# Kernel tuning notes

Hardware: AMD Instinct MI355X
Metric: run time of the kernel (lower is better)

## Reference

```python
import jax, jax.numpy as jnp
import numpy as np

D_MODEL = 1024
N_HEAD = 16
D_FF = 4 * D_MODEL
LN_EPS = 1e-5


def _layernorm(x, g, b):
    mu = jnp.mean(x, axis=-1, keepdims=True)
    var = jnp.mean(jnp.square(x - mu), axis=-1, keepdims=True)
    return (x - mu) * jax.lax.rsqrt(var + LN_EPS) * g + b


def _mha(q_in, k_in, v_in, mask, wq, bq, wk, wv, bv, wo, bo):
    B, Tq, D = q_in.shape
    H, Dk = N_HEAD, D // N_HEAD
    q = (q_in @ wq + bq).reshape(B, Tq, H, Dk).transpose(0, 2, 1, 3)      # [B,H,Tq,Dk]
    k = (k_in @ wk).reshape(B, -1, H, Dk).transpose(0, 2, 1, 3)           # [B,H,Tk,Dk]
    v = (v_in @ wv + bv).reshape(B, -1, H, Dk).transpose(0, 2, 1, 3)      # [B,H,Tk,Dk]
    attn = jnp.einsum('bhqd,bhkd->bhqk', q, k) / jnp.sqrt(jnp.float32(Dk))
    if mask is not None:
        m0 = (mask[:, None, :, :] == 0)                                    # [B,1,Tq,Tk]
        attn = jnp.where(m0, -jnp.inf, attn)
        attn = jax.nn.softmax(attn, axis=-1)
        attn = jnp.where(m0, 0.0, attn)
    else:
        attn = jax.nn.softmax(attn, axis=-1)
    out = jnp.einsum('bhqk,bhkd->bhqd', attn, v)
    out = out.transpose(0, 2, 1, 3).reshape(B, Tq, D)
    return out @ wo + bo


def setup_inputs() -> dict:
    key = jax.random.key(0)
    ks = jax.random.split(key, 32)
    B, T, S, D = 4, 1024, 1024, D_MODEL
    w = lambda k, shp: 0.02 * jax.random.normal(k, shp, dtype=jnp.float32)
    inp = {
        'dec_input': jax.random.normal(ks[0], (B, T, D), dtype=jnp.float32),
        'enc_output': jax.random.normal(ks[1], (B, S, D), dtype=jnp.float32),
        'self_mask': jnp.broadcast_to(jnp.tril(jnp.ones((T, T), jnp.int32)), (B, T, T)),
        'cross_mask': jnp.ones((B, T, S), jnp.int32),
        'sa_ln_g': jnp.ones((D,), jnp.float32), 'sa_ln_b': jnp.zeros((D,), jnp.float32),
        'sa_wq': w(ks[2], (D, D)), 'sa_bq': jnp.zeros((D,), jnp.float32),
        'sa_wk': w(ks[3], (D, D)),
        'sa_wv': w(ks[4], (D, D)), 'sa_bv': jnp.zeros((D,), jnp.float32),
        'sa_wo': w(ks[5], (D, D)), 'sa_bo': jnp.zeros((D,), jnp.float32),
        'ca_ln_g': jnp.ones((D,), jnp.float32), 'ca_ln_b': jnp.zeros((D,), jnp.float32),
        'ca_wq': w(ks[6], (D, D)), 'ca_bq': jnp.zeros((D,), jnp.float32),
        'ca_wk': w(ks[7], (D, D)),
        'ca_wv': w(ks[8], (D, D)), 'ca_bv': jnp.zeros((D,), jnp.float32),
        'ca_wo': w(ks[9], (D, D)), 'ca_bo': jnp.zeros((D,), jnp.float32),
        'mlp_ln_g': jnp.ones((D,), jnp.float32), 'mlp_ln_b': jnp.zeros((D,), jnp.float32),
        'w1': w(ks[10], (D, D_FF)), 'b1': jnp.zeros((D_FF,), jnp.float32),
        'w2': w(ks[11], (D_FF, D)), 'b2': jnp.zeros((D,), jnp.float32),
    }
    return inp


def reference(dec_input, enc_output, self_mask, cross_mask,
              sa_ln_g, sa_ln_b, sa_wq, sa_bq, sa_wk, sa_wv, sa_bv, sa_wo, sa_bo,
              ca_ln_g, ca_ln_b, ca_wq, ca_bq, ca_wk, ca_wv, ca_bv, ca_wo, ca_bo,
              mlp_ln_g, mlp_ln_b, w1, b1, w2, b2):
    # self-attention block (pre-norm, residual)
    x = _layernorm(dec_input, sa_ln_g, sa_ln_b)
    x = dec_input + _mha(x, x, x, self_mask, sa_wq, sa_bq, sa_wk, sa_wv, sa_bv, sa_wo, sa_bo)
    # cross-attention block
    h = _layernorm(x, ca_ln_g, ca_ln_b)
    x = x + _mha(h, enc_output, enc_output, cross_mask, ca_wq, ca_bq, ca_wk, ca_wv, ca_bv, ca_wo, ca_bo)
    # GELU FFN block
    h = _layernorm(x, mlp_ln_g, mlp_ln_b)
    x = x + (jax.nn.gelu(h @ w1 + b1, approximate=False) @ w2 + b2)
    return x
```

## Files before the change

### kernel.cpp

```cpp
#include <hip/hip_runtime.h>
#include <math.h>

typedef unsigned short u16;
typedef unsigned int   u32;
typedef __attribute__((ext_vector_type(8))) short bf16x8;
typedef __attribute__((ext_vector_type(4))) float f32x4;

__device__ __forceinline__ u16 f2bf(float f) {
  u32 u = __builtin_bit_cast(u32, f);
  u += 0x7fffu + ((u >> 16) & 1u);
  return (u16)(u >> 16);
}
__device__ __forceinline__ u32 cvtpk(float lo, float hi_) {
  u32 r;
  asm("v_cvt_pk_bf16_f32 %0, %1, %2" : "=v"(r) : "v"(lo), "v"(hi_));
  return r;
}
__device__ __forceinline__ float erf_fast(float x) {
  const float ax = fabsf(x);
  const float tt = 1.0f / fmaf(0.3275911f, ax, 1.0f);
  float p = fmaf(1.061405429f, tt, -1.453152027f);
  p = fmaf(p, tt, 1.421413741f);
  p = fmaf(p, tt, -0.284496736f);
  p = fmaf(p, tt, 0.254829592f);
  const float r = 1.0f - p * tt * __expf(-ax * ax);
  return copysignf(r, x);
}

__device__ __forceinline__ void g2l16(const u16* g, u16* l) {
  __builtin_amdgcn_global_load_lds(
      (const __attribute__((address_space(1))) unsigned int*)g,
      (__attribute__((address_space(3))) unsigned int*)l, 16, 0, 0);
}

struct TC8 { const float* s[8]; u16* d[8]; };
__global__ __launch_bounds__(256)
void transcvt8_kernel(TC8 p) {
  const float* __restrict__ W = p.s[blockIdx.z];
  u16* __restrict__ Wt = p.d[blockIdx.z];
  __shared__ float tile[32][33];
  const int n0 = blockIdx.x * 32, k0 = blockIdx.y * 32;
  const int tx = threadIdx.x & 31, ty = threadIdx.x >> 5;
  for (int i = 0; i < 4; ++i)
    tile[ty + 8 * i][tx] = W[(size_t)(k0 + ty + 8 * i) * 1024 + n0 + tx];
  __syncthreads();
  for (int i = 0; i < 4; ++i)
    Wt[(size_t)(n0 + ty + 8 * i) * 1024 + k0 + tx] = f2bf(tile[tx][ty + 8 * i]);
}

__global__ __launch_bounds__(256)
void transcvt_kernel(const float* __restrict__ W, u16* __restrict__ Wt, int K, int N) {
  __shared__ float tile[32][33];
  const int n0 = blockIdx.x * 32, k0 = blockIdx.y * 32;
  const int tx = threadIdx.x & 31, ty = threadIdx.x >> 5;
  for (int i = 0; i < 4; ++i)
    tile[ty + 8 * i][tx] = W[(size_t)(k0 + ty + 8 * i) * N + n0 + tx];
  __syncthreads();
  for (int i = 0; i < 4; ++i)
    Wt[(size_t)(n0 + ty + 8 * i) * K + k0 + tx] = f2bf(tile[tx][ty + 8 * i]);
}

__global__ __launch_bounds__(256)
void cvt_kernel(const float* __restrict__ in, u16* __restrict__ out) {
  const int i = blockIdx.x * 256 + threadIdx.x;
  const float4 v = ((const float4*)in)[i];
  u16 o[4] = {f2bf(v.x), f2bf(v.y), f2bf(v.z), f2bf(v.w)};
  ((ushort4*)out)[i] = *(ushort4*)o;
}

__global__ __launch_bounds__(256)
void pack_bias_kernel(const float* __restrict__ bq, const float* __restrict__ bv,
                      const float* __restrict__ cbv,
                      float* __restrict__ B3, float* __restrict__ B2) {
  const int i = blockIdx.x * 256 + threadIdx.x;
  if (i < 3072) {
    float v = 0.0f;
    if (i < 1024) v = bq[i];
    else if (i >= 2048) v = bv[i - 2048];
    B3[i] = v;
  } else {
    const int j = i - 3072;
    B2[j] = (j >= 1024) ? cbv[j - 1024] : 0.0f;
  }
}

__global__ __launch_bounds__(256)
void ln_kernel(const float* __restrict__ x, const float* __restrict__ g,
               const float* __restrict__ b, u16* __restrict__ out) {
  const int row = blockIdx.x;
  const float4 v4 = ((const float4*)(x + (size_t)row * 1024))[threadIdx.x];
  float vv[4] = {v4.x, v4.y, v4.z, v4.w};
  float s = vv[0] + vv[1] + vv[2] + vv[3];
  float s2 = vv[0] * vv[0] + vv[1] * vv[1] + vv[2] * vv[2] + vv[3] * vv[3];
  for (int m = 1; m < 64; m <<= 1) { s += __shfl_xor(s, m); s2 += __shfl_xor(s2, m); }
  __shared__ float ss[4], ss2[4];
  const int w = threadIdx.x >> 6;
  if ((threadIdx.x & 63) == 0) { ss[w] = s; ss2[w] = s2; }
  __syncthreads();
  s = ss[0] + ss[1] + ss[2] + ss[3];
  s2 = ss2[0] + ss2[1] + ss2[2] + ss2[3];
  const float mu = s * (1.0f / 1024.0f);
  const float var = s2 * (1.0f / 1024.0f) - mu * mu;
  const float r = rsqrtf(var + 1e-5f);
  const int c = threadIdx.x * 4;
  const float4 g4 = ((const float4*)g)[threadIdx.x];
  const float4 b4 = ((const float4*)b)[threadIdx.x];
  float gg[4] = {g4.x, g4.y, g4.z, g4.w};
  float bb[4] = {b4.x, b4.y, b4.z, b4.w};
  u16 o[4];
  for (int j = 0; j < 4; ++j) o[j] = f2bf((vv[j] - mu) * r * gg[j] + bb[j]);
  ((ushort4*)(out + (size_t)row * 1024 + c))[0] = *(ushort4*)o;
}

template<bool RES_F32, bool GELU>
__global__ __launch_bounds__(512)
void gemm_kernel(const u16* __restrict__ A, const u16* __restrict__ Bt,
                 const float* __restrict__ bias, const float* __restrict__ res,
                 void* __restrict__ Cout, int M, int N, int K) {
  __shared__ u16 As[3][128][64];
  __shared__ u16 Bs[3][128][64];
  const int t = threadIdx.x, lane = t & 63, w = t >> 6;
  const int wr = w >> 2, wc = w & 3;
  const int gx = gridDim.x;
  const int nwg = gx * gridDim.y;
  const int orig = blockIdx.y * gx + blockIdx.x;
  const int q8 = nwg >> 3;
  const int wgid = (orig & 7) * q8 + (orig >> 3);
  const int m0 = (wgid / gx) * 128, n0 = (wgid % gx) * 128;
  const int fr = lane & 15, fg = lane >> 4;
  const int srow = t >> 3;
  const int schunk = (t & 7) ^ (srow & 7);
  const u16* Ag = &A[(size_t)(m0 + srow) * K + schunk * 8];
  const u16* Bg = &Bt[(size_t)(n0 + srow) * K + schunk * 8];
  const size_t r64 = (size_t)64 * K;
  f32x4 acc[4][2] = {};
  #pragma unroll
  for (int ti0 = 0; ti0 < 2; ++ti0) {
    const size_t kk = (size_t)ti0 * 64;
    g2l16(Ag + kk,       &As[ti0][w * 8][0]);
    g2l16(Ag + r64 + kk, &As[ti0][64 + w * 8][0]);
    g2l16(Bg + kk,       &Bs[ti0][w * 8][0]);
    g2l16(Bg + r64 + kk, &Bs[ti0][64 + w * 8][0]);
  }
  const int nt = K >> 6;
  int c = 0;
  for (int ti = 0; ti < nt; ++ti) {
    if (ti + 1 < nt) asm volatile("s_waitcnt vmcnt(4)" ::: "memory");
    else             asm volatile("s_waitcnt vmcnt(0)" ::: "memory");
    __builtin_amdgcn_s_barrier();
    __builtin_amdgcn_sched_barrier(0);
    if (ti + 2 < nt) {
      const int nx = (c + 2 >= 3) ? c - 1 : c + 2;
      const size_t kn = (size_t)(ti + 2) * 64;
      g2l16(Ag + kn,       &As[nx][w * 8][0]);
      g2l16(Ag + r64 + kn, &As[nx][64 + w * 8][0]);
      g2l16(Bg + kn,       &Bs[nx][w * 8][0]);
      g2l16(Bg + r64 + kn, &Bs[nx][64 + w * 8][0]);
    }
    bf16x8 af[2][4], bfr[2][2];
    #pragma unroll
    for (int kk = 0; kk < 2; ++kk) {
      #pragma unroll
      for (int m = 0; m < 4; ++m) {
        const int row = wr * 64 + m * 16 + fr;
        af[kk][m] = *(bf16x8*)&As[c][row][((kk * 4 + fg) ^ (fr & 7)) * 8];
      }
      #pragma unroll
      for (int n = 0; n < 2; ++n) {
        const int row = wc * 32 + n * 16 + fr;
        bfr[kk][n] = *(bf16x8*)&Bs[c][row][((kk * 4 + fg) ^ (fr & 7)) * 8];
      }
    }
    __builtin_amdgcn_s_setprio(1);
    #pragma unroll
    for (int kk = 0; kk < 2; ++kk)
      #pragma unroll
      for (int m = 0; m < 4; ++m)
        #pragma unroll
        for (int n = 0; n < 2; ++n)
          acc[m][n] = __builtin_amdgcn_mfma_f32_16x16x32_bf16(af[kk][m], bfr[kk][n], acc[m][n], 0, 0, 0);
    __builtin_amdgcn_s_setprio(0);
    c = (c + 1 == 3) ? 0 : c + 1;
  }
  #pragma unroll
  for (int m = 0; m < 4; ++m)
    #pragma unroll
    for (int n = 0; n < 2; ++n) {
      const int col = n0 + wc * 32 + n * 16 + fr;
      const float bv = bias ? bias[col] : 0.0f;
      #pragma unroll
      for (int i = 0; i < 4; ++i) {
        const int row = m0 + wr * 64 + m * 16 + fg * 4 + i;
        float v = acc[m][n][i] + bv;
        if (GELU) v = 0.5f * v * (1.0f + erf_fast(v * 0.70710678118654752f));
        if (RES_F32)
          ((float*)Cout)[(size_t)row * N + col] = res[(size_t)row * N + col] + v;
        else
          ((u16*)Cout)[(size_t)row * N + col] = f2bf(v);
      }
    }
}

template<bool GELU>
__global__ __launch_bounds__(512, 2)
void gemm_big_kernel(const u16* __restrict__ A, const u16* __restrict__ Bt,
                     const float* __restrict__ bias, void* __restrict__ Cout,
                     int M, int N, int K) {
  __shared__ u16 As[2][256][64];
  __shared__ u16 Bs[2][256][64];
  const int t = threadIdx.x, lane = t & 63, w = t >> 6;
  const int wr = w >> 2, wc = w & 3;
  const int gx = gridDim.x;
  const int nwg = gx * gridDim.y;
  const int orig = blockIdx.y * gx + blockIdx.x;
  const int q8 = nwg >> 3;
  const int wgid = (orig & 7) * q8 + (orig >> 3);
  const int m0 = (wgid / gx) * 256, n0 = (wgid % gx) * 256;
  const int fr = lane & 15, fg = lane >> 4;
  const int srow = t >> 3;
  const int schunk = (t & 7) ^ (srow & 7);
  const u16* Ag = &A[(size_t)(m0 + srow) * K + schunk * 8];
  const u16* Bg = &Bt[(size_t)(n0 + srow) * K + schunk * 8];
  const size_t r64 = (size_t)64 * K;
  f32x4 acc[8][4] = {};
  #pragma unroll
  for (int i = 0; i < 4; ++i) {
    g2l16(Ag + i * r64, &As[0][i * 64 + w * 8][0]);
    g2l16(Bg + i * r64, &Bs[0][i * 64 + w * 8][0]);
  }
  const int nt = K >> 6;
  int c = 0;
  for (int ti = 0; ti < nt; ++ti) {
    __builtin_amdgcn_s_barrier();
    if (ti + 1 < nt) {
      const int nx = c ^ 1;
      const size_t kn = (size_t)(ti + 1) * 64;
      #pragma unroll
      for (int i = 0; i < 4; ++i) {
        g2l16(Ag + i * r64 + kn, &As[nx][i * 64 + w * 8][0]);
        g2l16(Bg + i * r64 + kn, &Bs[nx][i * 64 + w * 8][0]);
      }
      asm volatile("s_waitcnt vmcnt(8)" ::: "memory");
    } else {
      asm volatile("s_waitcnt vmcnt(0)" ::: "memory");
    }
    __builtin_amdgcn_s_barrier();
    __builtin_amdgcn_sched_barrier(0);
    #pragma unroll
    for (int kk = 0; kk < 2; ++kk) {
      bf16x8 af[8], bfr[4];
      #pragma unroll
      for (int m = 0; m < 8; ++m) {
        const int row = wr * 128 + m * 16 + fr;
        af[m] = *(bf16x8*)&As[c][row][((kk * 4 + fg) ^ (fr & 7)) * 8];
      }
      #pragma unroll
      for (int n = 0; n < 4; ++n) {
        const int row = wc * 64 + n * 16 + fr;
        bfr[n] = *(bf16x8*)&Bs[c][row][((kk * 4 + fg) ^ (fr & 7)) * 8];
      }
      __builtin_amdgcn_s_setprio(1);
      #pragma unroll
      for (int m = 0; m < 8; ++m)
        #pragma unroll
        for (int n = 0; n < 4; ++n)
          acc[m][n] = __builtin_amdgcn_mfma_f32_16x16x32_bf16(af[m], bfr[n], acc[m][n], 0, 0, 0);
      __builtin_amdgcn_s_setprio(0);
    }
    c ^= 1;
  }
  #pragma unroll
  for (int m = 0; m < 8; ++m)
    #pragma unroll
    for (int n = 0; n < 4; ++n) {
      const int col = n0 + wc * 64 + n * 16 + fr;
      const float bv = bias ? bias[col] : 0.0f;
      #pragma unroll
      for (int i = 0; i < 4; ++i) {
        const int row = m0 + wr * 128 + m * 16 + fg * 4 + i;
        float v = acc[m][n][i] + bv;
        if (GELU) v = 0.5f * v * (1.0f + erf_fast(v * 0.70710678118654752f));
        ((u16*)Cout)[(size_t)row * N + col] = f2bf(v);
      }
    }
}

template<bool CAUSAL>
__global__ __launch_bounds__(512)
void attn_kernel(const u16* __restrict__ Q, int ldq,
                 const u16* __restrict__ K, int ldk,
                 const u16* __restrict__ V, int ldv,
                 u16* __restrict__ O) {
  __shared__ u16 Ks[2][64][64];
  __shared__ u16 VsT[2][64][64];
  __shared__ u16 Ps[8][16][72];
  const int bh = blockIdx.x, b = bh >> 4, h = bh & 15;
  const int yy = blockIdx.y;
  const int qy = (yy & 1) ? ((yy - 1) >> 1) : (7 - (yy >> 1));
  const int t = threadIdx.x, w = t >> 6, lane = t & 63;
  const int ql = lane & 15;
  const int hi = lane >> 4;
  const int qr = qy * 128 + w * 16;
  const int qz = qr + ql;
  const int hcol = h * 64;
  const int nkt = CAUSAL ? 2 * qy + 2 : 16;
  const int wlim = CAUSAL ? (qr >> 6) : nkt - 1;
  const u16* Kb = K + (size_t)(b * 1024) * ldk + hcol;
  const u16* Vb = V + (size_t)(b * 1024) * ldv + hcol;
  const size_t qgrow = (size_t)(b * 1024 + qz) * ldq + hcol;
  const bf16x8 qb0 = *(const bf16x8*)&Q[qgrow + hi * 8];
  const bf16x8 qb1 = *(const bf16x8*)&Q[qgrow + 32 + hi * 8];
  f32x4 o[4] = {};
  float mrow = -1e30f, lsum = 0.0f;
  const u16* Ksrc = &Kb[(size_t)(t >> 3) * ldk + (size_t)(((t & 7) ^ ((t >> 3) & 7)) * 8)];
  const int sp = t >> 3, sm = t & 7;
  const float c1 = 0.125f * 1.44269504f;
  g2l16(Ksrc, &Ks[0][w * 8][0]);
  if (t < 256) {
    const bf16x8 va = *(const bf16x8*)&Vb[(size_t)(2 * sp) * ldv + 8 * sm];
    const bf16x8 vb = *(const bf16x8*)&Vb[(size_t)(2 * sp + 1) * ldv + 8 * sm];
    #pragma unroll
    for (int jj = 0; jj < 8; ++jj) {
      u32 pr = (u32)((const u16*)&va)[jj] | ((u32)((const u16*)&vb)[jj] << 16);
      *(u32*)&VsT[0][8 * sm + jj][(2 * sp) ^ ((jj ^ sm) << 3)] = pr;
    }
  }
  __syncthreads();

  for (int kt = 0; kt < nkt; ++kt) {
    const int cur = kt & 1, nx = cur ^ 1;
    const int k0 = kt * 64;
    bf16x8 va, vb;
    const bool havenext = (kt + 1 < nkt);
    if (havenext) {
      g2l16(Ksrc + (size_t)(k0 + 64) * ldk, &Ks[nx][w * 8][0]);
      if (t < 256) {
        va = *(const bf16x8*)&Vb[(size_t)(k0 + 64 + 2 * sp) * ldv + 8 * sm];
        vb = *(const bf16x8*)&Vb[(size_t)(k0 + 64 + 2 * sp + 1) * ldv + 8 * sm];
      }
    }
    if (kt <= wlim) {
      bf16x8 kf[8];
      const int sz = ql & 7;
      #pragma unroll
      for (int j = 0; j < 4; ++j) {
        kf[j]     = *(const bf16x8*)&Ks[cur][j * 16 + ql][(hi ^ sz) << 3];
        kf[4 + j] = *(const bf16x8*)&Ks[cur][j * 16 + ql][((hi + 4) ^ sz) << 3];
      }
      f32x4 s[4] = {};
      __builtin_amdgcn_s_setprio(1);
      #pragma unroll
      for (int j = 0; j < 4; ++j)
        s[j] = __builtin_amdgcn_mfma_f32_16x16x32_bf16(kf[j], qb0, s[j], 0, 0, 0);
      #pragma unroll
      for (int j = 0; j < 4; ++j)
        s[j] = __builtin_amdgcn_mfma_f32_16x16x32_bf16(kf[4 + j], qb1, s[j], 0, 0, 0);
      __builtin_amdgcn_s_setprio(0);
      float e2[4][4];
      float rm = -1e30f;
      const bool domask = CAUSAL && (kt == wlim);
      #pragma unroll
      for (int j = 0; j < 4; ++j)
        #pragma unroll
        for (int i = 0; i < 4; ++i) {
          float a = s[j][i] * c1;
          if (domask && (k0 + j * 16 + hi * 4 + i > qz)) a = -1e30f;
          e2[j][i] = a;
          rm = fmaxf(rm, a);
        }
      if (!__all(rm <= mrow + 8.0f)) {
        rm = fmaxf(rm, __shfl_xor(rm, 16));
        rm = fmaxf(rm, __shfl_xor(rm, 32));
        const float mn = fmaxf(mrow, rm);
        const float sc = exp2f(mrow - mn);
        lsum *= sc;
        float scv[4];
        #pragma unroll
        for (int i = 0; i < 4; ++i) scv[i] = __shfl(sc, hi * 4 + i);
        #pragma unroll
        for (int nb = 0; nb < 4; ++nb)
          #pragma unroll
          for (int i = 0; i < 4; ++i) o[nb][i] *= scv[i];
        mrow = mn;
      }
      float p[4][4];
      #pragma unroll
      for (int j = 0; j < 4; ++j)
        #pragma unroll
        for (int i = 0; i < 4; ++i) { p[j][i] = exp2f(e2[j][i] - mrow); lsum += p[j][i]; }
      #pragma unroll
      for (int j = 0; j < 4; ++j) {
        *(u32*)&Ps[w][ql][j * 16 + hi * 4]     = cvtpk(p[j][0], p[j][1]);
        *(u32*)&Ps[w][ql][j * 16 + hi * 4 + 2] = cvtpk(p[j][2], p[j][3]);
      }
      asm volatile("s_waitcnt lgkmcnt(0)" ::: "memory");
      __builtin_amdgcn_sched_barrier(0);
      const bf16x8 pa0 = *(const bf16x8*)&Ps[w][ql][hi * 8];
      const bf16x8 pa1 = *(const bf16x8*)&Ps[w][ql][32 + hi * 8];
      __builtin_amdgcn_s_setprio(1);
      #pragma unroll
      for (int nb = 0; nb < 4; ++nb) {
        const int dim = nb * 16 + ql;
        const int swz = ((dim & 7) ^ ((dim >> 3) & 7)) << 3;
        const bf16x8 v0 = *(const bf16x8*)&VsT[cur][dim][(hi * 8) ^ swz];
        const bf16x8 v1 = *(const bf16x8*)&VsT[cur][dim][(32 + hi * 8) ^ swz];
        o[nb] = __builtin_amdgcn_mfma_f32_16x16x32_bf16(pa0, v0, o[nb], 0, 0, 0);
        o[nb] = __builtin_amdgcn_mfma_f32_16x16x32_bf16(pa1, v1, o[nb], 0, 0, 0);
      }
      __builtin_amdgcn_s_setprio(0);
    }
    if (havenext && t < 256) {
      #pragma unroll
      for (int jj = 0; jj < 8; ++jj) {
        u32 pr = (u32)((const u16*)&va)[jj] | ((u32)((const u16*)&vb)[jj] << 16);
        *(u32*)&VsT[nx][8 * sm + jj][(2 * sp) ^ ((jj ^ sm) << 3)] = pr;
      }
    }
    __syncthreads();
  }

  float ltot = lsum + __shfl_xor(lsum, 16);
  ltot += __shfl_xor(ltot, 32);
  const float inv = 1.0f / ltot;
  #pragma unroll
  for (int i = 0; i < 4; ++i) {
    const float invq = __shfl(inv, hi * 4 + i);
    const size_t row = (size_t)(b * 1024 + qr + hi * 4 + i);
    #pragma unroll
    for (int nb = 0; nb < 4; ++nb)
      O[row * 1024 + hcol + nb * 16 + ql] = f2bf(o[nb][i] * invq);
  }
}

extern "C" void kernel_launch(void* const* d_in, const int* in_sizes, int n_in,
                              void* d_out, int out_size, void* d_ws, size_t ws_size,
                              hipStream_t stream) {
  const float* dec  = (const float*)d_in[0];
  const float* enc  = (const float*)d_in[1];
  const float* sa_g = (const float*)d_in[4];
  const float* sa_b = (const float*)d_in[5];
  const float* sa_wq = (const float*)d_in[6];
  const float* sa_bq = (const float*)d_in[7];
  const float* sa_wk = (const float*)d_in[8];
  const float* sa_wv = (const float*)d_in[9];
  const float* sa_bv = (const float*)d_in[10];
  const float* sa_wo = (const float*)d_in[11];
  const float* sa_bo = (const float*)d_in[12];
  const float* ca_g = (const float*)d_in[13];
  const float* ca_b = (const float*)d_in[14];
  const float* ca_wq = (const float*)d_in[15];
  const float* ca_bq = (const float*)d_in[16];
  const float* ca_wk = (const float*)d_in[17];
  const float* ca_wv = (const float*)d_in[18];
  const float* ca_bv = (const float*)d_in[19];
  const float* ca_wo = (const float*)d_in[20];
  const float* ca_bo = (const float*)d_in[21];
  const float* mlp_g = (const float*)d_in[22];
  const float* mlp_b = (const float*)d_in[23];
  const float* w1 = (const float*)d_in[24];
  const float* b1 = (const float*)d_in[25];
  const float* w2 = (const float*)d_in[26];
  const float* b2 = (const float*)d_in[27];

  const size_t MB = 1024 * 1024;
  if (ws_size < 97 * MB) return;
  char* ws = (char*)d_ws;
  u16* WQKV = (u16*)(ws + 0 * MB);
  u16* CQT  = (u16*)(ws + 6 * MB);
  u16* CKV  = (u16*)(ws + 8 * MB);
  u16* WOT  = (u16*)(ws + 12 * MB);
  u16* COT  = (u16*)(ws + 14 * MB);
  float* B3 = (float*)(ws + 16 * MB);
  float* B2 = (float*)(ws + 16 * MB + 16384);
  u16* XLN  = (u16*)(ws + 17 * MB);
  u16* AO   = (u16*)(ws + 25 * MB);
  u16* W1T  = (u16*)(ws + 25 * MB);
  u16* ENC  = (u16*)(ws + 33 * MB);
  u16* FB   = (u16*)(ws + 41 * MB);
  u16* EF   = (u16*)(ws + 41 * MB);
  u16* CQB  = (u16*)(ws + 57 * MB);
  u16* H1   = (u16*)(ws + 33 * MB);
  float* X1 = (float*)(ws + 65 * MB);
  u16* W2T  = (u16*)(ws + 65 * MB);
  float* X2 = (float*)(ws + 81 * MB);
  float* OUT = (float*)d_out;

  const dim3 blk(256), gblk(512), ablk(512);
  TC8 tc;
  tc.s[0] = sa_wq; tc.d[0] = WQKV;
  tc.s[1] = sa_wk; tc.d[1] = WQKV + 1024 * 1024;
  tc.s[2] = sa_wv; tc.d[2] = WQKV + 2048 * 1024;
  tc.s[3] = sa_wo; tc.d[3] = WOT;
  tc.s[4] = ca_wq; tc.d[4] = CQT;
  tc.s[5] = ca_wk; tc.d[5] = CKV;
  tc.s[6] = ca_wv; tc.d[6] = CKV + 1024 * 1024;
  tc.s[7] = ca_wo; tc.d[7] = COT;
  transcvt8_kernel<<<dim3(32, 32, 8), blk, 0, stream>>>(tc);
  pack_bias_kernel<<<dim3(20), blk, 0, stream>>>(sa_bq, sa_bv, ca_bv, B3, B2);
  cvt_kernel<<<dim3(4096), blk, 0, stream>>>(enc, ENC);

  ln_kernel<<<dim3(4096), blk, 0, stream>>>(dec, sa_g, sa_b, XLN);
  gemm_big_kernel<false><<<dim3(12, 16), gblk, 0, stream>>>(XLN, WQKV, B3, FB, 4096, 3072, 1024);
  attn_kernel<true><<<dim3(64, 8), ablk, 0, stream>>>(FB, 3072, FB + 1024, 3072, FB + 2048, 3072, AO);
  gemm_kernel<true, false><<<dim3(8, 32), gblk, 0, stream>>>(AO, WOT, sa_bo, dec, X1, 4096, 1024, 1024);

  ln_kernel<<<dim3(4096), blk, 0, stream>>>(X1, ca_g, ca_b, XLN);
  gemm_big_kernel<false><<<dim3(8, 16), gblk, 0, stream>>>(ENC, CKV, B2, EF, 4096, 2048, 1024);
  gemm_kernel<false, false><<<dim3(8, 32), gblk, 0, stream>>>(XLN, CQT, ca_bq, nullptr, CQB, 4096, 1024, 1024);
  attn_kernel<false><<<dim3(64, 8), ablk, 0, stream>>>(CQB, 1024, EF, 2048, EF + 1024, 2048, AO);
  gemm_kernel<true, false><<<dim3(8, 32), gblk, 0, stream>>>(AO, COT, ca_bo, X1, X2, 4096, 1024, 1024);

  transcvt_kernel<<<dim3(128, 32), blk, 0, stream>>>(w1, W1T, 1024, 4096);
  transcvt_kernel<<<dim3(32, 128), blk, 0, stream>>>(w2, W2T, 4096, 1024);
  ln_kernel<<<dim3(4096), blk, 0, stream>>>(X2, mlp_g, mlp_b, XLN);
  gemm_big_kernel<true><<<dim3(16, 16), gblk, 0, stream>>>(XLN, W1T, b1, H1, 4096, 4096, 1024);
  gemm_kernel<true, false><<<dim3(8, 32), gblk, 0, stream>>>(H1, W2T, b2, X2, OUT, 4096, 1024, 4096);
}
```

Baseline: 369.2 us.

## Restructure N=1024 GEMM to 4 waves with 64x64 warp tiles and double buffering

The 128x128-tile GEMM used for the output projections, cross-attention Q and FFN down-projection now runs 256 threads (4 waves, 2x2) instead of 512. Each wave computes a 64x64 sub-tile instead of 64x32, and LDS goes from triple to double buffering with the next-tile prefetch issued before the wait. The aim is more MFMA work per LDS fragment load, with two blocks per CU for occupancy. In exchange, each wave carries a larger accumulator and more register pressure, and the shallower prefetch pipeline may expose more global-load latency.

```diff
diff --git a/kernel.cpp b/kernel.cpp
--- a/kernel.cpp
+++ b/kernel.cpp
@@ -113,14 +113,14 @@
 }
 
 template<bool RES_F32, bool GELU>
-__global__ __launch_bounds__(512)
+__global__ __launch_bounds__(256, 2)
 void gemm_kernel(const u16* __restrict__ A, const u16* __restrict__ Bt,
                  const float* __restrict__ bias, const float* __restrict__ res,
                  void* __restrict__ Cout, int M, int N, int K) {
-  __shared__ u16 As[3][128][64];
-  __shared__ u16 Bs[3][128][64];
+  __shared__ u16 As[2][128][64];
+  __shared__ u16 Bs[2][128][64];
   const int t = threadIdx.x, lane = t & 63, w = t >> 6;
-  const int wr = w >> 2, wc = w & 3;
+  const int wr = w >> 1, wc = w & 1;
   const int gx = gridDim.x;
   const int nwg = gx * gridDim.y;
   const int orig = blockIdx.y * gx + blockIdx.x;
@@ -132,61 +132,59 @@
   const int schunk = (t & 7) ^ (srow & 7);
   const u16* Ag = &A[(size_t)(m0 + srow) * K + schunk * 8];
   const u16* Bg = &Bt[(size_t)(n0 + srow) * K + schunk * 8];
-  const size_t r64 = (size_t)64 * K;
-  f32x4 acc[4][2] = {};
+  const size_t r32 = (size_t)32 * K;
+  f32x4 acc[4][4] = {};
   #pragma unroll
-  for (int ti0 = 0; ti0 < 2; ++ti0) {
-    const size_t kk = (size_t)ti0 * 64;
-    g2l16(Ag + kk,       &As[ti0][w * 8][0]);
-    g2l16(Ag + r64 + kk, &As[ti0][64 + w * 8][0]);
-    g2l16(Bg + kk,       &Bs[ti0][w * 8][0]);
-    g2l16(Bg + r64 + kk, &Bs[ti0][64 + w * 8][0]);
+  for (int q = 0; q < 4; ++q) {
+    g2l16(Ag + q * r32, &As[0][q * 32 + w * 8][0]);
+    g2l16(Bg + q * r32, &Bs[0][q * 32 + w * 8][0]);
   }
   const int nt = K >> 6;
   int c = 0;
   for (int ti = 0; ti < nt; ++ti) {
-    if (ti + 1 < nt) asm volatile("s_waitcnt vmcnt(4)" ::: "memory");
-    else             asm volatile("s_waitcnt vmcnt(0)" ::: "memory");
+    __builtin_amdgcn_s_barrier();
+    if (ti + 1 < nt) {
+      const int nx = c ^ 1;
+      const size_t kn = (size_t)(ti + 1) * 64;
+      #pragma unroll
+      for (int q = 0; q < 4; ++q) {
+        g2l16(Ag + q * r32 + kn, &As[nx][q * 32 + w * 8][0]);
+        g2l16(Bg + q * r32 + kn, &Bs[nx][q * 32 + w * 8][0]);
+      }
+      asm volatile("s_waitcnt vmcnt(8)" ::: "memory");
+    } else {
+      asm volatile("s_waitcnt vmcnt(0)" ::: "memory");
+    }
     __builtin_amdgcn_s_barrier();
     __builtin_amdgcn_sched_barrier(0);
-    if (ti + 2 < nt) {
-      const int nx = (c + 2 >= 3) ? c - 1 : c + 2;
-      const size_t kn = (size_t)(ti + 2) * 64;
-      g2l16(Ag + kn,       &As[nx][w * 8][0]);
-      g2l16(Ag + r64 + kn, &As[nx][64 + w * 8][0]);
-      g2l16(Bg + kn,       &Bs[nx][w * 8][0]);
-      g2l16(Bg + r64 + kn, &Bs[nx][64 + w * 8][0]);
-    }
-    bf16x8 af[2][4], bfr[2][2];
     #pragma unroll
     for (int kk = 0; kk < 2; ++kk) {
+      bf16x8 af[4], bfr[4];
       #pragma unroll
       for (int m = 0; m < 4; ++m) {
         const int row = wr * 64 + m * 16 + fr;
-        af[kk][m] = *(bf16x8*)&As[c][row][((kk * 4 + fg) ^ (fr & 7)) * 8];
-      }
-      #pragma unroll
-      for (int n = 0; n < 2; ++n) {
-        const int row = wc * 32 + n * 16 + fr;
-        bfr[kk][n] = *(bf16x8*)&Bs[c][row][((kk * 4 + fg) ^ (fr & 7)) * 8];
-      }
-    }
-    __builtin_amdgcn_s_setprio(1);
-    #pragma unroll
-    for (int kk = 0; kk < 2; ++kk)
+        af[m] = *(bf16x8*)&As[c][row][((kk * 4 + fg) ^ (fr & 7)) * 8];
+      }
+      #pragma unroll
+      for (int n = 0; n < 4; ++n) {
+        const int row = wc * 64 + n * 16 + fr;
+        bfr[n] = *(bf16x8*)&Bs[c][row][((kk * 4 + fg) ^ (fr & 7)) * 8];
+      }
+      __builtin_amdgcn_s_setprio(1);
       #pragma unroll
       for (int m = 0; m < 4; ++m)
         #pragma unroll
-        for (int n = 0; n < 2; ++n)
-          acc[m][n] = __builtin_amdgcn_mfma_f32_16x16x32_bf16(af[kk][m], bfr[kk][n], acc[m][n], 0, 0, 0);
-    __builtin_amdgcn_s_setprio(0);
-    c = (c + 1 == 3) ? 0 : c + 1;
+        for (int n = 0; n < 4; ++n)
+          acc[m][n] = __builtin_amdgcn_mfma_f32_16x16x32_bf16(af[m], bfr[n], acc[m][n], 0, 0, 0);
+      __builtin_amdgcn_s_setprio(0);
+    }
+    c ^= 1;
   }
   #pragma unroll
   for (int m = 0; m < 4; ++m)
     #pragma unroll
-    for (int n = 0; n < 2; ++n) {
-      const int col = n0 + wc * 32 + n * 16 + fr;
+    for (int n = 0; n < 4; ++n) {
+      const int col = n0 + wc * 64 + n * 16 + fr;
       const float bv = bias ? bias[col] : 0.0f;
       #pragma unroll
       for (int i = 0; i < 4; ++i) {
@@ -485,7 +483,7 @@
   float* X2 = (float*)(ws + 81 * MB);
   float* OUT = (float*)d_out;
 
-  const dim3 blk(256), gblk(512), ablk(512);
+  const dim3 blk(256), gblk(512);
   TC8 tc;
   tc.s[0] = sa_wq; tc.d[0] = WQKV;
   tc.s[1] = sa_wk; tc.d[1] = WQKV + 1024 * 1024;
@@ -501,18 +499,18 @@
 
   ln_kernel<<<dim3(4096), blk, 0, stream>>>(dec, sa_g, sa_b, XLN);
   gemm_big_kernel<false><<<dim3(12, 16), gblk, 0, stream>>>(XLN, WQKV, B3, FB, 4096, 3072, 1024);
-  attn_kernel<true><<<dim3(64, 8), ablk, 0, stream>>>(FB, 3072, FB + 1024, 3072, FB + 2048, 3072, AO);
-  gemm_kernel<true, false><<<dim3(8, 32), gblk, 0, stream>>>(AO, WOT, sa_bo, dec, X1, 4096, 1024, 1024);
+  attn_kernel<true><<<dim3(64, 8), gblk, 0, stream>>>(FB, 3072, FB + 1024, 3072, FB + 2048, 3072, AO);
+  gemm_kernel<true, false><<<dim3(8, 32), blk, 0, stream>>>(AO, WOT, sa_bo, dec, X1, 4096, 1024, 1024);
 
   ln_kernel<<<dim3(4096), blk, 0, stream>>>(X1, ca_g, ca_b, XLN);
   gemm_big_kernel<false><<<dim3(8, 16), gblk, 0, stream>>>(ENC, CKV, B2, EF, 4096, 2048, 1024);
-  gemm_kernel<false, false><<<dim3(8, 32), gblk, 0, stream>>>(XLN, CQT, ca_bq, nullptr, CQB, 4096, 1024, 1024);
-  attn_kernel<false><<<dim3(64, 8), ablk, 0, stream>>>(CQB, 1024, EF, 2048, EF + 1024, 2048, AO);
-  gemm_kernel<true, false><<<dim3(8, 32), gblk, 0, stream>>>(AO, COT, ca_bo, X1, X2, 4096, 1024, 1024);
+  gemm_kernel<false, false><<<dim3(8, 32), blk, 0, stream>>>(XLN, CQT, ca_bq, nullptr, CQB, 4096, 1024, 1024);
+  attn_kernel<false><<<dim3(64, 8), gblk, 0, stream>>>(CQB, 1024, EF, 2048, EF + 1024, 2048, AO);
+  gemm_kernel<true, false><<<dim3(8, 32), blk, 0, stream>>>(AO, COT, ca_bo, X1, X2, 4096, 1024, 1024);
 
   transcvt_kernel<<<dim3(128, 32), blk, 0, stream>>>(w1, W1T, 1024, 4096);
   transcvt_kernel<<<dim3(32, 128), blk, 0, stream>>>(w2, W2T, 4096, 1024);
   ln_kernel<<<dim3(4096), blk, 0, stream>>>(X2, mlp_g, mlp_b, XLN);
   gemm_big_kernel<true><<<dim3(16, 16), gblk, 0, stream>>>(XLN, W1T, b1, H1, 4096, 4096, 1024);
-  gemm_kernel<true, false><<<dim3(8, 32), gblk, 0, stream>>>(H1, W2T, b2, X2, OUT, 4096, 1024, 4096);
-}
+  gemm_kernel<true, false><<<dim3(8, 32), blk, 0, stream>>>(H1, W2T, b2, X2, OUT, 4096, 1024, 4096);
+}
```

Result: slower. 384.4 us (+4.1%).
